# Performance work log

Measured on AMD Instinct MI355X. Metric: run time of the kernel, lower is better.

The kernel has to match this reference:

```python
import jax, jax.numpy as jnp
import numpy as np

HEADS = 4
DIM_HEAD = 32
SCALE = DIM_HEAD ** -0.5


def setup_inputs() -> dict:
    key = jax.random.key(0)
    k1, k2, k3 = jax.random.split(key, 3)
    dim, hidden = 256, HEADS * DIM_HEAD
    x = jax.random.normal(k1, (4, dim, 64, 64), dtype=jnp.float32)
    w_qkv = jax.random.normal(k2, (hidden * 3, dim), dtype=jnp.float32) * (dim ** -0.5)
    w_out = jax.random.normal(k3, (dim, hidden), dtype=jnp.float32) * (hidden ** -0.5)
    b_out = jnp.zeros((dim,), dtype=jnp.float32)
    return {"x": x, "w_qkv": w_qkv, "w_out": w_out, "b_out": b_out}


def reference(x, w_qkv, w_out, b_out):
    b, c, h, w = x.shape
    # 1x1 conv (no bias) == channel matmul
    qkv = jnp.einsum('bchw,oc->bohw', x, w_qkv)           # [b, 3*hidden, h, w]
    q, k, v = jnp.split(qkv, 3, axis=1)
    def to_heads(t):
        # [b, heads*d, h, w] -> [b, heads, h*w, d]
        return t.reshape(b, HEADS, DIM_HEAD, h * w).transpose(0, 1, 3, 2)
    q, k, v = to_heads(q) * SCALE, to_heads(k), to_heads(v)
    sim = jnp.einsum('bhid,bhjd->bhij', q, k)             # [b, heads, hw, hw]
    attn = jax.nn.softmax(sim, axis=-1)
    out = jnp.einsum('bhij,bhjd->bhid', attn, v)          # [b, heads, hw, d]
    out = out.transpose(0, 1, 3, 2).reshape(b, HEADS * DIM_HEAD, h, w)
    # output 1x1 conv with bias
    return jnp.einsum('bchw,oc->bohw', out, w_out) + b_out[None, :, None, None]
```

## Files before the change

### kernel.cpp

```cpp
#include <hip/hip_runtime.h>
#include <hip/hip_fp16.h>

#define HEADS 4
#define DH    32
#define HW    4096
#define CIN   256
#define HID   128

using half8   = __attribute__((ext_vector_type(8))) _Float16;
using half4   = __attribute__((ext_vector_type(4))) _Float16;
using half2v  = __attribute__((ext_vector_type(2))) _Float16;
using floatx4 = __attribute__((ext_vector_type(4))) float;

#define SHIFT2 4.328085122666891f
#define WQSCALE 0.25508275947f

static __device__ __forceinline__ half2v pk2(float a, float b) {
  return __builtin_bit_cast(half2v, __builtin_amdgcn_cvt_pkrtz(a, b));
}

__global__ __launch_bounds__(256) void qkv_fused(
    const float* __restrict__ w, const float* __restrict__ x,
    _Float16* __restrict__ Qw, _Float16* __restrict__ Kw,
    _Float16* __restrict__ Vtw)
{
  __shared__ float t[64][65];
  __shared__ _Float16 As[64][72];
  __shared__ _Float16 Bs[64][72];
  const int mt = blockIdx.x, nt = blockIdx.y;
  const int b = nt >> 6, p0 = (nt & 63) * 64;
  const int tid = threadIdx.x;
  const int wv = tid >> 6, lane = tid & 63, lm = lane & 15, quad = lane >> 4;
  const float wscale = (mt < 2) ? WQSCALE : 1.0f;

  const float* Ag = w + (size_t)(mt * 64) * CIN;
  const float* xb = x + (size_t)b * CIN * HW + p0;

  floatx4 acc[4] = {{0,0,0,0},{0,0,0,0},{0,0,0,0},{0,0,0,0}};

  for (int kq = 0; kq < 4; ++kq) {
    __syncthreads();
    #pragma unroll
    for (int i = 0; i < 4; ++i) {
      int ci = tid + i * 256;
      int cc = ci >> 4, p4 = (ci & 15) * 4;
      *(float4*)&t[cc][p4] =
          *(const float4*)(xb + (size_t)(kq * 64 + cc) * HW + p4);
    }
    #pragma unroll
    for (int i = 0; i < 2; ++i) {
      int ci = tid + i * 256;
      int r = ci >> 3, c8 = (ci & 7) * 8;
      const float* src = Ag + (size_t)r * CIN + kq * 64 + c8;
      float4 u0 = *(const float4*)(src);
      float4 u1 = *(const float4*)(src + 4);
      half8 h = {(_Float16)(u0.x * wscale), (_Float16)(u0.y * wscale),
                 (_Float16)(u0.z * wscale), (_Float16)(u0.w * wscale),
                 (_Float16)(u1.x * wscale), (_Float16)(u1.y * wscale),
                 (_Float16)(u1.z * wscale), (_Float16)(u1.w * wscale)};
      *(half8*)&As[r][c8] = h;
    }
    __syncthreads();
    #pragma unroll
    for (int i = 0; i < 2; ++i) {
      int idx = tid + i * 256;
      int p = idx >> 3, c0 = (idx & 7) * 8;
      half8 v;
      #pragma unroll
      for (int k = 0; k < 8; ++k) v[k] = (_Float16)t[c0 + k][p];
      *(half8*)&Bs[p][c0] = v;
    }
    __syncthreads();
    #pragma unroll
    for (int ks = 0; ks < 2; ++ks) {
      half8 a = *(const half8*)&As[wv * 16 + lm][ks * 32 + quad * 8];
      #pragma unroll
      for (int ns = 0; ns < 4; ++ns) {
        half8 bf = *(const half8*)&Bs[ns * 16 + lm][ks * 32 + quad * 8];
        acc[ns] = __builtin_amdgcn_mfma_f32_16x16x32_f16(a, bf, acc[ns], 0, 0, 0);
      }
    }
  }

  const int sec = mt >> 1;
  const int o_base = (mt & 1) * 64 + wv * 16 + quad * 4;
  const int hh = o_base >> 5, dd = o_base & 31;
  const int bh = b * HEADS + hh;
  if (sec < 2) {
    _Float16* dst = (sec == 0) ? Qw : Kw;
    #pragma unroll
    for (int ns = 0; ns < 4; ++ns) {
      int p = p0 + ns * 16 + lm;
      half4 v = {(_Float16)acc[ns][0], (_Float16)acc[ns][1],
                 (_Float16)acc[ns][2], (_Float16)acc[ns][3]};
      *(half4*)(dst + ((size_t)bh * HW + p) * DH + dd) = v;
    }
  } else {
    #pragma unroll
    for (int ns = 0; ns < 4; ++ns) {
      int p = p0 + ns * 16 + lm;
      #pragma unroll
      for (int r = 0; r < 4; ++r)
        Vtw[((size_t)bh * DH + dd + r) * HW + p] = (_Float16)acc[ns][r];
    }
  }
}

__global__ __launch_bounds__(256) void attn(
    const _Float16* __restrict__ Qw, const _Float16* __restrict__ Kw,
    const _Float16* __restrict__ Vtw, _Float16* __restrict__ Ot)
{
  __shared__ _Float16 ks[2][2][64][40];
  __shared__ _Float16 vt[2][2][32][74];

  const int bh = blockIdx.y, qt = blockIdx.x;
  const int tid = threadIdx.x;
  const int wv = tid >> 6, lane = tid & 63, lm = lane & 15, quad = lane >> 4;

  const _Float16* qbase =
      Qw + ((size_t)bh * HW + qt * 128 + wv * 16 + lm) * DH + quad * 8;
  const half8 qa0 = *(const half8*)qbase;
  const half8 qa1 = *(const half8*)(qbase + (size_t)64 * DH);

  const _Float16 one = (_Float16)1.0f;
  const half4 ones4 = {one, one, one, one};
  const floatx4 shiftc = {-SHIFT2, -SHIFT2, -SHIFT2, -SHIFT2};

  floatx4 oT[2][2] = {{{0,0,0,0},{0,0,0,0}},{{0,0,0,0},{0,0,0,0}}};
  floatx4 l4[2]    = {{0,0,0,0},{0,0,0,0}};

  const _Float16* kbase = Kw  + (size_t)bh * HW * DH;
  const _Float16* vbase = Vtw + (size_t)bh * DH * HW;
  const int kr = tid >> 2, kc = (tid & 3) * 8;
  const int vr = tid >> 3, vc = (tid & 7) * 8;

  half8 kA = *(const half8*)(kbase + (size_t)kr * DH + kc);
  half8 vA = *(const half8*)(vbase + (size_t)vr * HW + vc);
  half8 kB = *(const half8*)(kbase + ((size_t)64 + kr) * DH + kc);
  half8 vB = *(const half8*)(vbase + (size_t)vr * HW + 64 + vc);
  *(half8*)&ks[0][0][kr][kc] = kA;
  *(half8*)&vt[0][0][vr][vc] = vA;
  *(half8*)&ks[0][1][kr][kc] = kB;
  *(half8*)&vt[0][1][vr][vc] = vB;
  kA = *(const half8*)(kbase + ((size_t)128 + kr) * DH + kc);
  vA = *(const half8*)(vbase + (size_t)vr * HW + 128 + vc);
  kB = *(const half8*)(kbase + ((size_t)192 + kr) * DH + kc);
  vB = *(const half8*)(vbase + (size_t)vr * HW + 192 + vc);
  __syncthreads();

  for (int it = 0; it < HW / 128; ++it) {
    const int ph = it & 1, nx = ph ^ 1;

    half8 kf[2][4];
    half4 vf[2][4][2];
    #pragma unroll
    for (int sub = 0; sub < 2; ++sub) {
      #pragma unroll
      for (int f = 0; f < 4; ++f) {
        kf[sub][f]    = *(const half8*)&ks[ph][sub][f * 16 + lm][quad * 8];
        vf[sub][f][0] = *(const half4*)&vt[ph][sub][lm][f * 16 + quad * 4];
        vf[sub][f][1] = *(const half4*)&vt[ph][sub][16 + lm][f * 16 + quad * 4];
      }
    }

    *(half8*)&ks[nx][0][kr][kc] = kA;
    *(half8*)&vt[nx][0][vr][vc] = vA;
    *(half8*)&ks[nx][1][kr][kc] = kB;
    *(half8*)&vt[nx][1][vr][vc] = vB;
    size_t koff = (size_t)(it * 2 + 4) * 64;
    if (koff > HW - 128) koff = HW - 128;
    kA = *(const half8*)(kbase + (koff + kr) * DH + kc);
    vA = *(const half8*)(vbase + (size_t)vr * HW + koff + vc);
    kB = *(const half8*)(kbase + (koff + 64 + kr) * DH + kc);
    vB = *(const half8*)(vbase + (size_t)vr * HW + koff + 64 + vc);

    #pragma unroll
    for (int sub = 0; sub < 2; ++sub) {
      #pragma unroll
      for (int f = 0; f < 4; ++f) {
        floatx4 sT0 = __builtin_amdgcn_mfma_f32_16x16x32_f16(kf[sub][f], qa0, shiftc, 0, 0, 0);
        floatx4 sT1 = __builtin_amdgcn_mfma_f32_16x16x32_f16(kf[sub][f], qa1, shiftc, 0, 0, 0);
        half2v a0 = pk2(__builtin_amdgcn_exp2f(sT0[0]), __builtin_amdgcn_exp2f(sT0[1]));
        half2v b0 = pk2(__builtin_amdgcn_exp2f(sT0[2]), __builtin_amdgcn_exp2f(sT0[3]));
        half2v a1 = pk2(__builtin_amdgcn_exp2f(sT1[0]), __builtin_amdgcn_exp2f(sT1[1]));
        half2v b1 = pk2(__builtin_amdgcn_exp2f(sT1[2]), __builtin_amdgcn_exp2f(sT1[3]));
        half4 pb0 = {a0.x, a0.y, b0.x, b0.y};
        half4 pb1 = {a1.x, a1.y, b1.x, b1.y};
        l4[0] = __builtin_amdgcn_mfma_f32_16x16x16f16(ones4, pb0, l4[0], 0, 0, 0);
        l4[1] = __builtin_amdgcn_mfma_f32_16x16x16f16(ones4, pb1, l4[1], 0, 0, 0);
        #pragma unroll
        for (int g = 0; g < 2; ++g) {
          oT[0][g] = __builtin_amdgcn_mfma_f32_16x16x16f16(vf[sub][f][g], pb0, oT[0][g], 0, 0, 0);
          oT[1][g] = __builtin_amdgcn_mfma_f32_16x16x16f16(vf[sub][f][g], pb1, oT[1][g], 0, 0, 0);
        }
      }
    }
    __syncthreads();
  }

  const int b = bh >> 2, hh = bh & 3;
  #pragma unroll
  for (int t = 0; t < 2; ++t) {
    const float inv = 1.0f / l4[t][0];
    _Float16* obase = Ot +
        ((size_t)(b * HW + qt * 128 + t * 64 + wv * 16 + lm)) * HID + hh * DH;
    #pragma unroll
    for (int g = 0; g < 2; ++g) {
      half4 v = {(_Float16)(oT[t][g][0] * inv), (_Float16)(oT[t][g][1] * inv),
                 (_Float16)(oT[t][g][2] * inv), (_Float16)(oT[t][g][3] * inv)};
      *(half4*)(obase + g * 16 + quad * 4) = v;
    }
  }
}

__global__ __launch_bounds__(256) void out_gemm(
    const float* __restrict__ wo, const _Float16* __restrict__ Ot,
    const float* __restrict__ bo, float* __restrict__ out)
{
  __shared__ _Float16 As[64][136];
  __shared__ _Float16 Bs[64][136];
  __shared__ float os[64][68];
  const int mt = blockIdx.x, nt = blockIdx.y;
  const int b = nt >> 6, p0 = (nt & 63) * 64;
  const int tid = threadIdx.x;
  const int wv = tid >> 6, lane = tid & 63, lm = lane & 15, quad = lane >> 4;

  const float* Ag = wo + (size_t)(mt * 64) * HID;
  const _Float16* B = Ot + ((size_t)b * HW + p0) * HID;

  #pragma unroll
  for (int i = 0; i < 4; ++i) {
    int ci = tid + i * 256;
    int r = ci >> 4, c8 = (ci & 15) * 8;
    const float* src = Ag + (size_t)r * HID + c8;
    float4 u0 = *(const float4*)(src);
    float4 u1 = *(const float4*)(src + 4);
    half8 h = {(_Float16)u0.x, (_Float16)u0.y, (_Float16)u0.z, (_Float16)u0.w,
               (_Float16)u1.x, (_Float16)u1.y, (_Float16)u1.z, (_Float16)u1.w};
    *(half8*)&As[r][c8] = h;
    *(half8*)&Bs[r][c8] = *(const half8*)(B + (size_t)r * HID + c8);
  }
  __syncthreads();

  floatx4 acc[4] = {{0,0,0,0},{0,0,0,0},{0,0,0,0},{0,0,0,0}};
  #pragma unroll
  for (int ks = 0; ks < 4; ++ks) {
    half8 a = *(const half8*)&As[wv * 16 + lm][ks * 32 + quad * 8];
    #pragma unroll
    for (int ns = 0; ns < 4; ++ns) {
      half8 bf = *(const half8*)&Bs[ns * 16 + lm][ks * 32 + quad * 8];
      acc[ns] = __builtin_amdgcn_mfma_f32_16x16x32_f16(a, bf, acc[ns], 0, 0, 0);
    }
  }

  #pragma unroll
  for (int ns = 0; ns < 4; ++ns)
    #pragma unroll
    for (int r = 0; r < 4; ++r)
      os[wv * 16 + quad * 4 + r][ns * 16 + lm] = acc[ns][r];
  __syncthreads();

  const int o = tid >> 2, pq = (tid & 3) * 16;
  const float bias = bo[mt * 64 + o];
  float* dst = out + ((size_t)(b * CIN + mt * 64 + o)) * HW + p0 + pq;
  #pragma unroll
  for (int j = 0; j < 4; ++j) {
    float4 v = *(const float4*)&os[o][pq + j * 4];
    v.x += bias; v.y += bias; v.z += bias; v.w += bias;
    *(float4*)(dst + j * 4) = v;
  }
}

extern "C" void kernel_launch(void* const* d_in, const int* in_sizes, int n_in,
                              void* d_out, int out_size, void* d_ws, size_t ws_size,
                              hipStream_t stream)
{
  const float* x     = (const float*)d_in[0];
  const float* w_qkv = (const float*)d_in[1];
  const float* w_out = (const float*)d_in[2];
  const float* b_out = (const float*)d_in[3];
  float* out = (float*)d_out;

  char* ws = (char*)d_ws;
  _Float16* Ot  = (_Float16*)(ws);
  _Float16* Qw  = (_Float16*)(ws + (8u  << 20));
  _Float16* Kw  = (_Float16*)(ws + (12u << 20));
  _Float16* Vtw = (_Float16*)(ws + (16u << 20));

  dim3 blk(256);
  qkv_fused<<<dim3(6, 256), blk, 0, stream>>>(w_qkv, x, Qw, Kw, Vtw);
  attn<<<dim3(32, 16), blk, 0, stream>>>(Qw, Kw, Vtw, Ot);
  out_gemm<<<dim3(4, 256), blk, 0, stream>>>(w_out, Ot, b_out, out);
}
```

Baseline: 163.1 us.

## Split attention over key dimension and reduce partials in output GEMM

Splits the key/value sequence into two halves via a third grid dimension, so twice as many attention blocks run. Each half writes unnormalized fp32 output partials and row sums. The output GEMM sums the partials and normalizes them while loading. This exploits the fixed softmax shift, which makes the partials additive, to raise occupancy. The cost is much more intermediate memory traffic, from fp32 partials that are reread by each output tile.

```diff
diff --git a/kernel.cpp b/kernel.cpp
--- a/kernel.cpp
+++ b/kernel.cpp
@@ -6,6 +6,8 @@
 #define HW    4096
 #define CIN   256
 #define HID   128
+#define KSPLIT 2
+#define KHALF (HW / KSPLIT)
 
 using half8   = __attribute__((ext_vector_type(8))) _Float16;
 using half4   = __attribute__((ext_vector_type(4))) _Float16;
@@ -108,12 +110,13 @@
 
 __global__ __launch_bounds__(256) void attn(
     const _Float16* __restrict__ Qw, const _Float16* __restrict__ Kw,
-    const _Float16* __restrict__ Vtw, _Float16* __restrict__ Ot)
+    const _Float16* __restrict__ Vtw, float* __restrict__ Op,
+    float* __restrict__ lp)
 {
   __shared__ _Float16 ks[2][2][64][40];
   __shared__ _Float16 vt[2][2][32][74];
 
-  const int bh = blockIdx.y, qt = blockIdx.x;
+  const int bh = blockIdx.y, qt = blockIdx.x, z = blockIdx.z;
   const int tid = threadIdx.x;
   const int wv = tid >> 6, lane = tid & 63, lm = lane & 15, quad = lane >> 4;
 
@@ -129,8 +132,8 @@
   floatx4 oT[2][2] = {{{0,0,0,0},{0,0,0,0}},{{0,0,0,0},{0,0,0,0}}};
   floatx4 l4[2]    = {{0,0,0,0},{0,0,0,0}};
 
-  const _Float16* kbase = Kw  + (size_t)bh * HW * DH;
-  const _Float16* vbase = Vtw + (size_t)bh * DH * HW;
+  const _Float16* kbase = Kw  + (size_t)bh * HW * DH + (size_t)z * KHALF * DH;
+  const _Float16* vbase = Vtw + (size_t)bh * DH * HW + (size_t)z * KHALF;
   const int kr = tid >> 2, kc = (tid & 3) * 8;
   const int vr = tid >> 3, vc = (tid & 7) * 8;
 
@@ -148,7 +151,7 @@
   vB = *(const half8*)(vbase + (size_t)vr * HW + 192 + vc);
   __syncthreads();
 
-  for (int it = 0; it < HW / 128; ++it) {
+  for (int it = 0; it < KHALF / 128; ++it) {
     const int ph = it & 1, nx = ph ^ 1;
 
     half8 kf[2][4];
@@ -168,7 +171,7 @@
     *(half8*)&ks[nx][1][kr][kc] = kB;
     *(half8*)&vt[nx][1][vr][vc] = vB;
     size_t koff = (size_t)(it * 2 + 4) * 64;
-    if (koff > HW - 128) koff = HW - 128;
+    if (koff > KHALF - 128) koff = KHALF - 128;
     kA = *(const half8*)(kbase + (koff + kr) * DH + kc);
     vA = *(const half8*)(vbase + (size_t)vr * HW + koff + vc);
     kB = *(const half8*)(kbase + (koff + 64 + kr) * DH + kc);
@@ -201,32 +204,43 @@
   const int b = bh >> 2, hh = bh & 3;
   #pragma unroll
   for (int t = 0; t < 2; ++t) {
-    const float inv = 1.0f / l4[t][0];
-    _Float16* obase = Ot +
-        ((size_t)(b * HW + qt * 128 + t * 64 + wv * 16 + lm)) * HID + hh * DH;
+    const int row = qt * 128 + t * 64 + wv * 16 + lm;
+    float* obase = Op +
+        ((size_t)z * 4 * HW + (size_t)b * HW + row) * HID + hh * DH;
     #pragma unroll
     for (int g = 0; g < 2; ++g) {
-      half4 v = {(_Float16)(oT[t][g][0] * inv), (_Float16)(oT[t][g][1] * inv),
-                 (_Float16)(oT[t][g][2] * inv), (_Float16)(oT[t][g][3] * inv)};
-      *(half4*)(obase + g * 16 + quad * 4) = v;
-    }
+      float4 v = {oT[t][g][0], oT[t][g][1], oT[t][g][2], oT[t][g][3]};
+      *(float4*)(obase + g * 16 + quad * 4) = v;
+    }
+    if (quad == 0)
+      lp[(size_t)z * HEADS * 4 * HW + (size_t)bh * HW + row] = l4[t][0];
   }
 }
 
 __global__ __launch_bounds__(256) void out_gemm(
-    const float* __restrict__ wo, const _Float16* __restrict__ Ot,
-    const float* __restrict__ bo, float* __restrict__ out)
+    const float* __restrict__ wo, const float* __restrict__ Op,
+    const float* __restrict__ lp, const float* __restrict__ bo,
+    float* __restrict__ out)
 {
   __shared__ _Float16 As[64][136];
   __shared__ _Float16 Bs[64][136];
   __shared__ float os[64][68];
+  __shared__ float inv_l[64][4];
   const int mt = blockIdx.x, nt = blockIdx.y;
   const int b = nt >> 6, p0 = (nt & 63) * 64;
   const int tid = threadIdx.x;
   const int wv = tid >> 6, lane = tid & 63, lm = lane & 15, quad = lane >> 4;
 
-  const float* Ag = wo + (size_t)(mt * 64) * HID;
-  const _Float16* B = Ot + ((size_t)b * HW + p0) * HID;
+  {
+    const int p = tid >> 2, hh = tid & 3;
+    const size_t qi = (size_t)(b * HEADS + hh) * HW + p0 + p;
+    inv_l[p][hh] = 1.0f / (lp[qi] + lp[(size_t)HEADS * 4 * HW + qi]);
+  }
+  __syncthreads();
+
+  const float* Ag  = wo + (size_t)(mt * 64) * HID;
+  const float* Bp0 = Op + ((size_t)b * HW + p0) * HID;
+  const float* Bp1 = Bp0 + (size_t)4 * HW * HID;
 
   #pragma unroll
   for (int i = 0; i < 4; ++i) {
@@ -238,7 +252,19 @@
     half8 h = {(_Float16)u0.x, (_Float16)u0.y, (_Float16)u0.z, (_Float16)u0.w,
                (_Float16)u1.x, (_Float16)u1.y, (_Float16)u1.z, (_Float16)u1.w};
     *(half8*)&As[r][c8] = h;
-    *(half8*)&Bs[r][c8] = *(const half8*)(B + (size_t)r * HID + c8);
+
+    const float* s0 = Bp0 + (size_t)r * HID + c8;
+    const float* s1 = Bp1 + (size_t)r * HID + c8;
+    float4 o0 = *(const float4*)(s0);
+    float4 o1 = *(const float4*)(s0 + 4);
+    float4 o2 = *(const float4*)(s1);
+    float4 o3 = *(const float4*)(s1 + 4);
+    const float sc = inv_l[r][c8 >> 5];
+    half8 hb = {(_Float16)((o0.x + o2.x) * sc), (_Float16)((o0.y + o2.y) * sc),
+                (_Float16)((o0.z + o2.z) * sc), (_Float16)((o0.w + o2.w) * sc),
+                (_Float16)((o1.x + o3.x) * sc), (_Float16)((o1.y + o3.y) * sc),
+                (_Float16)((o1.z + o3.z) * sc), (_Float16)((o1.w + o3.w) * sc)};
+    *(half8*)&Bs[r][c8] = hb;
   }
   __syncthreads();
 
@@ -282,13 +308,14 @@
   float* out = (float*)d_out;
 
   char* ws = (char*)d_ws;
-  _Float16* Ot  = (_Float16*)(ws);
-  _Float16* Qw  = (_Float16*)(ws + (8u  << 20));
-  _Float16* Kw  = (_Float16*)(ws + (12u << 20));
-  _Float16* Vtw = (_Float16*)(ws + (16u << 20));
+  _Float16* Qw  = (_Float16*)(ws);
+  _Float16* Kw  = (_Float16*)(ws + (4u  << 20));
+  _Float16* Vtw = (_Float16*)(ws + (8u  << 20));
+  float*    Op  = (float*)   (ws + (12u << 20));
+  float*    lp  = (float*)   (ws + (28u << 20));
 
   dim3 blk(256);
   qkv_fused<<<dim3(6, 256), blk, 0, stream>>>(w_qkv, x, Qw, Kw, Vtw);
-  attn<<<dim3(32, 16), blk, 0, stream>>>(Qw, Kw, Vtw, Ot);
-  out_gemm<<<dim3(4, 256), blk, 0, stream>>>(w_out, Ot, b_out, out);
-}
+  attn<<<dim3(32, 16, KSPLIT), blk, 0, stream>>>(Qw, Kw, Vtw, Op, lp);
+  out_gemm<<<dim3(4, 256), blk, 0, stream>>>(w_out, Op, lp, b_out, out);
+}
```

Measured after the change: 167.3 us. +2.6%, slower.
